# Optimization experiments

Measured on AMD Instinct MI355X. Metric: run time of the kernel, lower is better.

Reference implementation:

```python
import jax, jax.numpy as jnp
import numpy as np

# Dims from init_kwargs / input_specs
C_IN, H, W = 128, 224, 224
C_OUT, KH, KW = 256, 3, 3
STRIDE = 1  # padding='valid'


def setup_inputs() -> dict:
    key = jax.random.key(0)
    k1, k2 = jax.random.split(key)
    x = jax.random.normal(k1, (C_IN, H, W), dtype=jnp.float32)
    kernels = jax.random.normal(k2, (C_OUT, C_IN, KH, KW), dtype=jnp.float32) * 0.05
    return {"x": x, "kernels": kernels}


def reference(x, kernels):
    # Original does im2col + matmul, which is exactly a valid cross-correlation
    # (no kernel flip). Express it as a direct conv: (1,C,H,W) * (O,I,kh,kw).
    out = jax.lax.conv_general_dilated(
        x[None],                      # (1, C_in, H, W)
        kernels,                      # (C_out, C_in, KH, KW)
        window_strides=(STRIDE, STRIDE),
        padding="VALID",
        dimension_numbers=("NCHW", "OIHW", "NCHW"),
    )
    return out[0]                     # (C_out, H_out, W_out) = (256, 222, 222)
```

## Files before the change

### kernel.cpp

```cpp
#include <hip/hip_runtime.h>

#define CIN   128
#define HH    224
#define WW    224
#define COUT  256
#define HO    222
#define WO    222
#define PLANE (224 * 224 * 64)

typedef unsigned short u16;
typedef unsigned int   u32;
typedef __bf16  bf16x8 __attribute__((ext_vector_type(8)));
typedef float   f32x4  __attribute__((ext_vector_type(4)));

__device__ __forceinline__ u16 f2bf(float f) {
  union { float f; u32 u; } v; v.f = f;
  u32 u = v.u;
  return (u16)((u + 0x7FFFu + ((u >> 16) & 1u)) >> 16);
}

__global__ void pack_w(const float* __restrict__ w, u16* __restrict__ wp) {
  int b   = blockIdx.x * 256 + threadIdx.x;
  int jcp = b & 7;
  int r1  = b >> 3;
  int mr  = r1 & 127;
  int r2  = r1 >> 7;
  int ch  = r2 & 1;
  int r3  = r2 >> 1;
  int khw = r3 % 9;
  int mt  = r3 / 9;
  int jsrc  = jcp ^ (mr & 7);
  int oc    = mt * 128 + mr;
  int cbase = ch * 64 + jsrc * 8;
  u16 o[8];
#pragma unroll
  for (int e = 0; e < 8; ++e)
    o[e] = f2bf(w[(size_t)(oc * CIN + cbase + e) * 9 + khw]);
  uint4 v;
  v.x = (u32)o[0] | ((u32)o[1] << 16);
  v.y = (u32)o[2] | ((u32)o[3] << 16);
  v.z = (u32)o[4] | ((u32)o[5] << 16);
  v.w = (u32)o[6] | ((u32)o[7] << 16);
  *(uint4*)(&wp[(size_t)b * 8]) = v;
}

__global__ void pack_x(const float* __restrict__ x, u16* __restrict__ xp) {
  int h  = blockIdx.x;
  int ch = blockIdx.y;
  __shared__ u16 tile[64][226];
  int t = threadIdx.x;
#pragma unroll
  for (int i = 0; i < 14; ++i) {
    int idx = i * 256 + t;
    int c   = idx / 56;
    int wq  = idx % 56;
    float4 v = *(const float4*)(&x[(size_t)(ch * 64 + c) * (HH * WW) + h * WW + wq * 4]);
    tile[c][wq * 4 + 0] = f2bf(v.x);
    tile[c][wq * 4 + 1] = f2bf(v.y);
    tile[c][wq * 4 + 2] = f2bf(v.z);
    tile[c][wq * 4 + 3] = f2bf(v.w);
  }
  __syncthreads();
#pragma unroll
  for (int i = 0; i < 7; ++i) {
    int idx  = i * 256 + t;
    int w    = idx >> 3;
    int jcp  = idx & 7;
    int jsrc = jcp ^ (w & 7);
    u16 o[8];
#pragma unroll
    for (int e = 0; e < 8; ++e) o[e] = tile[jsrc * 8 + e][w];
    uint4 v;
    v.x = (u32)o[0] | ((u32)o[1] << 16);
    v.y = (u32)o[2] | ((u32)o[3] << 16);
    v.z = (u32)o[4] | ((u32)o[5] << 16);
    v.w = (u32)o[6] | ((u32)o[7] << 16);
    *(uint4*)(&xp[(size_t)ch * PLANE + (size_t)(h * WW + w) * 64 + jcp * 8]) = v;
  }
}

__device__ __forceinline__ void lds_dma16(const u16* g, u16* l) {
  __builtin_amdgcn_global_load_lds(
      reinterpret_cast<__attribute__((address_space(1))) u32*>(
          reinterpret_cast<uintptr_t>(g)),
      reinterpret_cast<__attribute__((address_space(3))) u32*>(
          reinterpret_cast<uintptr_t>(l)),
      16, 0, 0);
}

__global__ __launch_bounds__(256, 3) void conv_mfma(const u16* __restrict__ wp,
                                                    const u16* __restrict__ xp,
                                                    float* __restrict__ out) {
  __shared__ u16 ldsA[128 * 64];
  __shared__ u16 ldsB[128 * 64];

  const int tid    = threadIdx.x;
  const int lane   = tid & 63;
  const int wave   = tid >> 6;
  const int quad   = lane >> 4;
  const int lr     = lane & 15;
  const int wave_m = wave >> 1;
  const int wave_n = wave & 1;

  const int nb      = blockIdx.x;
  const int mt      = blockIdx.y;
  const int oh      = blockIdx.z;
  const int ow_base = nb * 94;

  f32x4 acc[4][4];
#pragma unroll
  for (int i = 0; i < 4; ++i)
#pragma unroll
    for (int j = 0; j < 4; ++j) acc[i][j] = {0.f, 0.f, 0.f, 0.f};

  int rowA[4], rowB[4];
#pragma unroll
  for (int i = 0; i < 4; ++i) {
    rowA[i] = (wave_m * 64 + i * 16 + lr) * 64;
    rowB[i] = (wave_n * 64 + i * 16 + lr) * 64;
  }
  const int m7  = lr & 7;
  const int stg = wave * 2048 + lane * 8;

  for (int it = 0; it < 18; ++it) {
    const int ch = it & 1;
    const int t2 = it >> 1;
    const int kw = t2 % 3;
    const int kh = t2 / 3;

    const u16* Ag = wp + (size_t)((mt * 9 + t2) * 2 + ch) * 8192;
    const u16* Bg = xp + (size_t)ch * PLANE +
                    (size_t)((oh + kh) * WW + ow_base + kw) * 64;

    __syncthreads();
#pragma unroll
    for (int i = 0; i < 4; ++i) {
      lds_dma16(Ag + stg + i * 512, &ldsA[wave * 2048 + i * 512]);
      lds_dma16(Bg + stg + i * 512, &ldsB[wave * 2048 + i * 512]);
    }
    __syncthreads();

    const int wb7 = (ow_base + kw + lr) & 7;

#pragma unroll
    for (int ks = 0; ks < 2; ++ks) {
      const int jc = ks * 4 + quad;
      bf16x8 af[4], bg[4];
#pragma unroll
      for (int i = 0; i < 4; ++i)
        af[i] = *reinterpret_cast<const bf16x8*>(&ldsA[rowA[i] + ((jc ^ m7) << 3)]);
#pragma unroll
      for (int i = 0; i < 4; ++i)
        bg[i] = *reinterpret_cast<const bf16x8*>(&ldsB[rowB[i] + ((jc ^ wb7) << 3)]);
#pragma unroll
      for (int i = 0; i < 4; ++i)
#pragma unroll
        for (int j = 0; j < 4; ++j)
          acc[i][j] = __builtin_amdgcn_mfma_f32_16x16x32_bf16(af[i], bg[j], acc[i][j], 0, 0, 0);
    }
  }

  const int m_base = mt * 128 + wave_m * 64;
  const int n_base = ow_base + wave_n * 64;
#pragma unroll
  for (int i = 0; i < 4; ++i) {
#pragma unroll
    for (int j = 0; j < 4; ++j) {
      float* op = out + (size_t)(m_base + i * 16 + quad * 4) * (HO * WO) +
                  (size_t)oh * WO + (n_base + j * 16 + lr);
#pragma unroll
      for (int r = 0; r < 4; ++r)
        op[(size_t)r * (HO * WO)] = acc[i][j][r];
    }
  }
}

__global__ void conv_naive(const float* __restrict__ x, const float* __restrict__ w,
                           float* __restrict__ out) {
  int idx = blockIdx.x * 256 + threadIdx.x;
  if (idx >= COUT * HO * WO) return;
  int ow  = idx % WO;
  int tmp = idx / WO;
  int oh  = tmp % HO;
  int oc  = tmp / HO;
  float s = 0.f;
  for (int c = 0; c < CIN; ++c)
    for (int kh = 0; kh < 3; ++kh) {
      const float* xr = &x[(size_t)(c * HH + oh + kh) * WW + ow];
      const float* wr = &w[((size_t)(oc * CIN + c) * 3 + kh) * 3];
      s += xr[0] * wr[0] + xr[1] * wr[1] + xr[2] * wr[2];
    }
  out[idx] = s;
}

extern "C" void kernel_launch(void* const* d_in, const int* in_sizes, int n_in,
                              void* d_out, int out_size, void* d_ws, size_t ws_size,
                              hipStream_t stream) {
  const float* x    = (const float*)d_in[0];
  const float* kern = (const float*)d_in[1];
  float* out        = (float*)d_out;

  const size_t WP_BYTES = (size_t)36864 * 16;
  const size_t XP_BYTES = (size_t)2 * PLANE * 2;

  if (ws_size >= WP_BYTES + XP_BYTES) {
    u16* wp = (u16*)d_ws;
    u16* xp = (u16*)((char*)d_ws + WP_BYTES);
    hipLaunchKernelGGL(pack_w, dim3(144), dim3(256), 0, stream, kern, wp);
    hipLaunchKernelGGL(pack_x, dim3(224, 2), dim3(256), 0, stream, x, xp);
    hipLaunchKernelGGL(conv_mfma, dim3(2, 2, 222), dim3(256), 0, stream, wp, xp, out);
  } else {
    int total = COUT * HO * WO;
    hipLaunchKernelGGL(conv_naive, dim3((total + 255) / 256), dim3(256), 0, stream,
                       x, kern, out);
  }
}
```

Baseline: 126.0 us.

## Stage full input row once per kh and reuse across kw, read weights from global

Restructures the conv kernel so each block covers a full output row (224 columns) for 128 output channels. Per (kh, channel-half) step it DMAs one whole input row into LDS and reuses it for all three kw shifts, while weight fragments are loaded straight from global/L2 instead of through LDS. The two packing kernels are merged into one prep launch, and the per-block tile grows to 4x7 MFMA tiles with occupancy lowered to 2. The intent is to cut redundant input loads and barriers, at the cost of more register pressure, uncoalesced global weight reads in the inner loop, and wasted columns past 222.

```diff
diff --git a/kernel.cpp b/kernel.cpp
--- a/kernel.cpp
+++ b/kernel.cpp
@@ -19,63 +19,61 @@
   return (u16)((u + 0x7FFFu + ((u >> 16) & 1u)) >> 16);
 }
 
-__global__ void pack_w(const float* __restrict__ w, u16* __restrict__ wp) {
-  int b   = blockIdx.x * 256 + threadIdx.x;
-  int jcp = b & 7;
-  int r1  = b >> 3;
-  int mr  = r1 & 127;
-  int r2  = r1 >> 7;
-  int ch  = r2 & 1;
-  int r3  = r2 >> 1;
-  int khw = r3 % 9;
-  int mt  = r3 / 9;
-  int jsrc  = jcp ^ (mr & 7);
-  int oc    = mt * 128 + mr;
-  int cbase = ch * 64 + jsrc * 8;
-  u16 o[8];
-#pragma unroll
-  for (int e = 0; e < 8; ++e)
-    o[e] = f2bf(w[(size_t)(oc * CIN + cbase + e) * 9 + khw]);
-  uint4 v;
-  v.x = (u32)o[0] | ((u32)o[1] << 16);
-  v.y = (u32)o[2] | ((u32)o[3] << 16);
-  v.z = (u32)o[4] | ((u32)o[5] << 16);
-  v.w = (u32)o[6] | ((u32)o[7] << 16);
-  *(uint4*)(&wp[(size_t)b * 8]) = v;
-}
-
-__global__ void pack_x(const float* __restrict__ x, u16* __restrict__ xp) {
-  int h  = blockIdx.x;
-  int ch = blockIdx.y;
-  __shared__ u16 tile[64][226];
-  int t = threadIdx.x;
-#pragma unroll
-  for (int i = 0; i < 14; ++i) {
-    int idx = i * 256 + t;
-    int c   = idx / 56;
-    int wq  = idx % 56;
-    float4 v = *(const float4*)(&x[(size_t)(ch * 64 + c) * (HH * WW) + h * WW + wq * 4]);
-    tile[c][wq * 4 + 0] = f2bf(v.x);
-    tile[c][wq * 4 + 1] = f2bf(v.y);
-    tile[c][wq * 4 + 2] = f2bf(v.z);
-    tile[c][wq * 4 + 3] = f2bf(v.w);
-  }
-  __syncthreads();
-#pragma unroll
-  for (int i = 0; i < 7; ++i) {
-    int idx  = i * 256 + t;
-    int w    = idx >> 3;
-    int jcp  = idx & 7;
-    int jsrc = jcp ^ (w & 7);
+__global__ void prep(const float* __restrict__ x, const float* __restrict__ w,
+                     u16* __restrict__ xp, u16* __restrict__ wp) {
+  const int t = threadIdx.x;
+  if (blockIdx.x < 448) {
+    const int h  = blockIdx.x >> 1;
+    const int ch = blockIdx.x & 1;
+    __shared__ u16 tile[64][228];
+#pragma unroll
+    for (int i = 0; i < 14; ++i) {
+      int idx = i * 256 + t;
+      int c   = idx / 56;
+      int wq  = idx % 56;
+      float4 v = *(const float4*)(&x[(size_t)(ch * 64 + c) * (HH * WW) + h * WW + wq * 4]);
+      uint2 p;
+      p.x = (u32)f2bf(v.x) | ((u32)f2bf(v.y) << 16);
+      p.y = (u32)f2bf(v.z) | ((u32)f2bf(v.w) << 16);
+      *(uint2*)(&tile[c][wq * 4]) = p;
+    }
+    __syncthreads();
+#pragma unroll
+    for (int i = 0; i < 7; ++i) {
+      int idx  = i * 256 + t;
+      int ww   = idx >> 3;
+      int jcp  = idx & 7;
+      int jsrc = jcp ^ (ww & 7);
+      uint4 v;
+      v.x = (u32)tile[jsrc * 8 + 0][ww] | ((u32)tile[jsrc * 8 + 1][ww] << 16);
+      v.y = (u32)tile[jsrc * 8 + 2][ww] | ((u32)tile[jsrc * 8 + 3][ww] << 16);
+      v.z = (u32)tile[jsrc * 8 + 4][ww] | ((u32)tile[jsrc * 8 + 5][ww] << 16);
+      v.w = (u32)tile[jsrc * 8 + 6][ww] | ((u32)tile[jsrc * 8 + 7][ww] << 16);
+      *(uint4*)(&xp[(size_t)ch * PLANE + (size_t)(h * WW + ww) * 64 + jcp * 8]) = v;
+    }
+  } else {
+    int u    = (blockIdx.x - 448) * 256 + t;
+    int jcp  = u & 7;
+    int mr   = (u >> 3) & 127;
+    int rest = u >> 10;
+    int kw   = rest % 3;
+    int q    = rest / 3;
+    int ch   = q & 1;
+    int r    = q >> 1;
+    int kh   = r % 3;
+    int mt   = r / 3;
+    int oc   = mt * 128 + mr;
+    int cb   = ch * 64 + (jcp ^ (mr & 7)) * 8;
     u16 o[8];
 #pragma unroll
-    for (int e = 0; e < 8; ++e) o[e] = tile[jsrc * 8 + e][w];
+    for (int e = 0; e < 8; ++e)
+      o[e] = f2bf(w[((size_t)(oc * CIN + cb + e) * 3 + kh) * 3 + kw]);
     uint4 v;
     v.x = (u32)o[0] | ((u32)o[1] << 16);
     v.y = (u32)o[2] | ((u32)o[3] << 16);
     v.z = (u32)o[4] | ((u32)o[5] << 16);
     v.w = (u32)o[6] | ((u32)o[7] << 16);
-    *(uint4*)(&xp[(size_t)ch * PLANE + (size_t)(h * WW + w) * 64 + jcp * 8]) = v;
+    *(uint4*)(&wp[(size_t)u * 8]) = v;
   }
 }
 
@@ -88,89 +86,85 @@
       16, 0, 0);
 }
 
-__global__ __launch_bounds__(256, 3) void conv_mfma(const u16* __restrict__ wp,
+__global__ __launch_bounds__(256, 2) void conv_mfma(const u16* __restrict__ wp,
                                                     const u16* __restrict__ xp,
                                                     float* __restrict__ out) {
-  __shared__ u16 ldsA[128 * 64];
-  __shared__ u16 ldsB[128 * 64];
-
-  const int tid    = threadIdx.x;
-  const int lane   = tid & 63;
-  const int wave   = tid >> 6;
-  const int quad   = lane >> 4;
-  const int lr     = lane & 15;
-  const int wave_m = wave >> 1;
-  const int wave_n = wave & 1;
-
-  const int nb      = blockIdx.x;
-  const int mt      = blockIdx.y;
-  const int oh      = blockIdx.z;
-  const int ow_base = nb * 94;
-
-  f32x4 acc[4][4];
+  __shared__ u16 ldsB[226 * 64];
+
+  const int tid  = threadIdx.x;
+  const int lane = tid & 63;
+  const int wave = tid >> 6;
+  const int quad = lane >> 4;
+  const int lr   = lane & 15;
+  const int wm   = wave >> 1;
+  const int wn   = wave & 1;
+
+  const int oh = blockIdx.x;
+  const int mt = blockIdx.y;
+
+  f32x4 acc[4][7];
 #pragma unroll
   for (int i = 0; i < 4; ++i)
 #pragma unroll
-    for (int j = 0; j < 4; ++j) acc[i][j] = {0.f, 0.f, 0.f, 0.f};
-
-  int rowA[4], rowB[4];
+    for (int j = 0; j < 7; ++j) acc[i][j] = {0.f, 0.f, 0.f, 0.f};
+
+  int swA[2];
+#pragma unroll
+  for (int ks = 0; ks < 2; ++ks)
+    swA[ks] = ((ks * 4 + quad) ^ (lr & 7)) << 3;
+
+  for (int s = 0; s < 6; ++s) {
+    const int ch = s & 1;
+    const int kh = s >> 1;
+
+    const u16* g = xp + (size_t)ch * PLANE + (size_t)(oh + kh) * (WW * 64);
+
+    __syncthreads();
+#pragma unroll
+    for (int uu = 0; uu < 7; ++uu) {
+      const int unit = wave * 7 + uu;
+      lds_dma16(g + unit * 512 + lane * 8, &ldsB[unit * 512]);
+    }
+    __syncthreads();
+
+    const u16* Ab = wp + (size_t)((mt * 3 + kh) * 2 + ch) * 24576 + wm * 4096 + lr * 64;
+
+#pragma unroll
+    for (int kw = 0; kw < 3; ++kw) {
+      const int bq  = (wn * 112 + lr + kw) * 64;
+      const int sw7 = (lr + kw) & 7;
+#pragma unroll
+      for (int ks = 0; ks < 2; ++ks) {
+        const int swB = ((ks * 4 + quad) ^ sw7) << 3;
+        bf16x8 af[4], bg[7];
+#pragma unroll
+        for (int i = 0; i < 4; ++i)
+          af[i] = *reinterpret_cast<const bf16x8*>(Ab + kw * 8192 + i * 1024 + swA[ks]);
+#pragma unroll
+        for (int j = 0; j < 7; ++j)
+          bg[j] = *reinterpret_cast<const bf16x8*>(&ldsB[bq + j * 1024 + swB]);
+#pragma unroll
+        for (int i = 0; i < 4; ++i)
+#pragma unroll
+          for (int j = 0; j < 7; ++j)
+            acc[i][j] = __builtin_amdgcn_mfma_f32_16x16x32_bf16(af[i], bg[j], acc[i][j], 0, 0, 0);
+      }
+    }
+  }
+
+  const int mb = mt * 128 + wm * 64;
 #pragma unroll
   for (int i = 0; i < 4; ++i) {
-    rowA[i] = (wave_m * 64 + i * 16 + lr) * 64;
-    rowB[i] = (wave_n * 64 + i * 16 + lr) * 64;
-  }
-  const int m7  = lr & 7;
-  const int stg = wave * 2048 + lane * 8;
-
-  for (int it = 0; it < 18; ++it) {
-    const int ch = it & 1;
-    const int t2 = it >> 1;
-    const int kw = t2 % 3;
-    const int kh = t2 / 3;
-
-    const u16* Ag = wp + (size_t)((mt * 9 + t2) * 2 + ch) * 8192;
-    const u16* Bg = xp + (size_t)ch * PLANE +
-                    (size_t)((oh + kh) * WW + ow_base + kw) * 64;
-
-    __syncthreads();
-#pragma unroll
-    for (int i = 0; i < 4; ++i) {
-      lds_dma16(Ag + stg + i * 512, &ldsA[wave * 2048 + i * 512]);
-      lds_dma16(Bg + stg + i * 512, &ldsB[wave * 2048 + i * 512]);
-    }
-    __syncthreads();
-
-    const int wb7 = (ow_base + kw + lr) & 7;
-
-#pragma unroll
-    for (int ks = 0; ks < 2; ++ks) {
-      const int jc = ks * 4 + quad;
-      bf16x8 af[4], bg[4];
-#pragma unroll
-      for (int i = 0; i < 4; ++i)
-        af[i] = *reinterpret_cast<const bf16x8*>(&ldsA[rowA[i] + ((jc ^ m7) << 3)]);
-#pragma unroll
-      for (int i = 0; i < 4; ++i)
-        bg[i] = *reinterpret_cast<const bf16x8*>(&ldsB[rowB[i] + ((jc ^ wb7) << 3)]);
-#pragma unroll
-      for (int i = 0; i < 4; ++i)
-#pragma unroll
-        for (int j = 0; j < 4; ++j)
-          acc[i][j] = __builtin_amdgcn_mfma_f32_16x16x32_bf16(af[i], bg[j], acc[i][j], 0, 0, 0);
-    }
-  }
-
-  const int m_base = mt * 128 + wave_m * 64;
-  const int n_base = ow_base + wave_n * 64;
-#pragma unroll
-  for (int i = 0; i < 4; ++i) {
-#pragma unroll
-    for (int j = 0; j < 4; ++j) {
-      float* op = out + (size_t)(m_base + i * 16 + quad * 4) * (HO * WO) +
-                  (size_t)oh * WO + (n_base + j * 16 + lr);
-#pragma unroll
-      for (int r = 0; r < 4; ++r)
-        op[(size_t)r * (HO * WO)] = acc[i][j][r];
+#pragma unroll
+    for (int j = 0; j < 7; ++j) {
+      const int col = wn * 112 + j * 16 + lr;
+      if (col < WO) {
+        float* op = out + (size_t)(mb + i * 16 + quad * 4) * (HO * WO) +
+                    (size_t)oh * WO + col;
+#pragma unroll
+        for (int r = 0; r < 4; ++r)
+          op[(size_t)r * (HO * WO)] = acc[i][j][r];
+      }
     }
   }
 }
@@ -206,9 +200,8 @@
   if (ws_size >= WP_BYTES + XP_BYTES) {
     u16* wp = (u16*)d_ws;
     u16* xp = (u16*)((char*)d_ws + WP_BYTES);
-    hipLaunchKernelGGL(pack_w, dim3(144), dim3(256), 0, stream, kern, wp);
-    hipLaunchKernelGGL(pack_x, dim3(224, 2), dim3(256), 0, stream, x, xp);
-    hipLaunchKernelGGL(conv_mfma, dim3(2, 2, 222), dim3(256), 0, stream, wp, xp, out);
+    hipLaunchKernelGGL(prep, dim3(592), dim3(256), 0, stream, x, kern, xp, wp);
+    hipLaunchKernelGGL(conv_mfma, dim3(222, 2), dim3(256), 0, stream, wp, xp, out);
   } else {
     int total = COUT * HO * WO;
     hipLaunchKernelGGL(conv_naive, dim3((total + 255) / 256), dim3(256), 0, stream,
```

Measured after the change: 122.7 us. 1.03x faster.
